# Kernel optimization log

Measured on AMD Instinct MI355X. Metric: run time of the kernel, lower is better.

The kernel has to match this reference:

```python
import jax, jax.numpy as jnp
import numpy as np

D_MODEL, D_STATE, D_CONV, EXPAND, L = 512, 16, 4, 2, 2048
D_INNER = EXPAND * D_MODEL


def _dwconv_causal(x, w, b):
    # x: (L, D), w: (D, K), b: (D,). torch Conv1d(groups=D, padding=K-1)[..., :L]
    K = w.shape[1]
    xp = jnp.pad(x, ((K - 1, 0), (0, 0)))
    windows = jnp.stack([xp[k:k + x.shape[0]] for k in range(K)], axis=-1)  # (L, D, K)
    return jnp.einsum('ldk,dk->ld', windows, w) + b


def _ssm_dir(x, inW, inb, cw, cb, xpW, xpb, dtW, dtb, outW, outb, A_log, Dp):
    xz = x @ inW + inb                      # (L, 2*Di)
    x_ssm, z = xz[:, :D_INNER], xz[:, D_INNER:]
    x_ssm = _dwconv_causal(x_ssm, cw, cb)   # (L, Di)
    sp = jax.nn.silu(x_ssm) @ xpW + xpb     # (L, Di + 2*S)
    delta = sp[:, :D_INNER]
    B = sp[:, D_INNER:D_INNER + D_STATE]
    C = sp[:, D_INNER + D_STATE:]
    dt = jax.nn.softplus(delta @ dtW + dtb)  # (L, Di)
    A = -jnp.exp(A_log)                      # (Di, S)
    dA = jnp.exp(dt[:, :, None] * A[None])                      # (L, Di, S)
    dBu = dt[:, :, None] * B[:, None, :] * x_ssm[:, :, None]    # (L, Di, S)

    def step(h, inp):
        a, bu = inp
        h = a * h + bu
        return h, h

    h0 = jnp.zeros((D_INNER, D_STATE), x.dtype)
    _, hs = jax.lax.scan(step, h0, (dA, dBu))   # (L, Di, S)
    y = jnp.einsum('lds,ls->ld', hs, C) + Dp * x_ssm
    return (y * jax.nn.silu(z)) @ outW + outb


def _make_params(key):
    ks = jax.random.split(key, 32)
    i = iter(range(32))
    def w(shape, scale=0.02):
        return (jax.random.normal(ks[next(i)], shape, jnp.float32) * scale)
    p = {}
    for pre in ('fwd_', 'bwd_'):
        p[pre + 'in_W'] = w((D_MODEL, 2 * D_INNER))
        p[pre + 'in_b'] = w((2 * D_INNER,))
        p[pre + 'conv_w'] = w((D_INNER, D_CONV), 0.1)
        p[pre + 'conv_b'] = w((D_INNER,))
        p[pre + 'xp_W'] = w((D_INNER, D_INNER + 2 * D_STATE))
        p[pre + 'xp_b'] = w((D_INNER + 2 * D_STATE,))
        p[pre + 'dt_W'] = w((D_INNER, D_INNER))
        p[pre + 'dt_b'] = w((D_INNER,))
        p[pre + 'out_W'] = w((D_INNER, D_MODEL))
        p[pre + 'out_b'] = w((D_MODEL,))
    p['A_log'] = jax.random.normal(ks[next(i)], (D_INNER, D_STATE), jnp.float32) * 0.5
    p['D_param'] = jnp.ones((D_INNER,), jnp.float32)
    p['fusion_W'] = w((2 * D_MODEL, D_MODEL))
    p['fusion_b'] = w((D_MODEL,))
    return p


def setup_inputs() -> dict:
    key = jax.random.key(0)
    kx, kp = jax.random.split(key)
    inp = {'x': jax.random.normal(kx, (L, D_MODEL), jnp.float32)}
    inp.update(_make_params(kp))
    return inp


def reference(x,
              fwd_in_W, fwd_in_b, fwd_conv_w, fwd_conv_b, fwd_xp_W, fwd_xp_b,
              fwd_dt_W, fwd_dt_b, fwd_out_W, fwd_out_b,
              bwd_in_W, bwd_in_b, bwd_conv_w, bwd_conv_b, bwd_xp_W, bwd_xp_b,
              bwd_dt_W, bwd_dt_b, bwd_out_W, bwd_out_b,
              A_log, D_param, fusion_W, fusion_b):
    out_fwd = _ssm_dir(x, fwd_in_W, fwd_in_b, fwd_conv_w, fwd_conv_b,
                       fwd_xp_W, fwd_xp_b, fwd_dt_W, fwd_dt_b,
                       fwd_out_W, fwd_out_b, A_log, D_param)
    out_bwd = _ssm_dir(x[::-1], bwd_in_W, bwd_in_b, bwd_conv_w, bwd_conv_b,
                       bwd_xp_W, bwd_xp_b, bwd_dt_W, bwd_dt_b,
                       bwd_out_W, bwd_out_b, A_log, D_param)[::-1]
    return jnp.concatenate([out_fwd, out_bwd], axis=-1) @ fusion_W + fusion_b
```

## Files before the change

kernel.cpp:

```cpp
#include <hip/hip_runtime.h>
#include <cmath>

#define L_SEQ 2048
#define DM 512
#define DI 1024
#define DS 16
#define NSP 1056
#define NC 64
#define CL 32

typedef unsigned short ushortT;
typedef unsigned int u32;
typedef __attribute__((ext_vector_type(8))) short short8;
typedef __attribute__((ext_vector_type(4))) float float4_t;
typedef __attribute__((address_space(1))) u32 gu32;
typedef __attribute__((address_space(3))) u32 lu32;

__device__ __forceinline__ float sigm(float x) { return 1.0f / (1.0f + __expf(-x)); }

__device__ __forceinline__ ushortT f2bf(float f) {
    unsigned u = __float_as_uint(f);
    unsigned r = u + 0x7FFFu + ((u >> 16) & 1u);
    return (ushortT)(r >> 16);
}

__device__ __forceinline__ void gl2lds16(const ushortT* g, ushortT* l) {
    __builtin_amdgcn_global_load_lds((gu32*)g, (lu32*)l, 16, 0, 0);
}

struct WC {
    const float* src[11];
    ushortT* dst[11];
    int ss[11], soff[11], ds_[11], tN[11], mode[11];
    int off[12];
};

__global__ __launch_bounds__(256) void wcvt_all(WC wc)
{
    __shared__ ushortT t[32][33];
    int b = blockIdx.x;
    int m = 0;
    while (b >= wc.off[m + 1]) ++m;
    int tl = b - wc.off[m];
    int n0 = (tl % wc.tN[m]) * 32;
    int k0 = (tl / wc.tN[m]) * 32;
    const float* W = wc.src[m];
    ushortT* D = wc.dst[m];
    int ss = wc.ss[m], soff = wc.soff[m], ds = wc.ds_[m];
    int tx = threadIdx.x & 31, ty = threadIdx.x >> 5;
    if (wc.mode[m] == 1) {
        #pragma unroll
        for (int i = 0; i < 32; i += 8)
            D[(size_t)(k0 + ty + i) * ds + n0 + tx] =
                f2bf(W[(size_t)(k0 + ty + i) * ss + soff + n0 + tx]);
    } else {
        #pragma unroll
        for (int i = 0; i < 32; i += 8)
            t[ty + i][tx] = f2bf(W[(size_t)(k0 + ty + i) * ss + soff + n0 + tx]);
        __syncthreads();
        #pragma unroll
        for (int i = 0; i < 32; i += 8)
            D[(size_t)(n0 + ty + i) * ds + k0 + tx] = t[tx][ty + i];
    }
}

__global__ __launch_bounds__(256) void bias_fold(
    const float* __restrict__ xpb0, const float* __restrict__ xpb1,
    const float* __restrict__ dtW0, const float* __restrict__ dtW1,
    const float* __restrict__ dtb0, const float* __restrict__ dtb1,
    const float* __restrict__ outb0, const float* __restrict__ outb1,
    const float* __restrict__ fuW, const float* __restrict__ fub,
    float* __restrict__ BFdt0, float* __restrict__ BFdt1, float* __restrict__ BFof)
{
    int idx = blockIdx.x * 256 + threadIdx.x;
    if (idx < 2112) {
        int dir = idx >= 1056;
        int m = idx - dir * 1056;
        const float* xpb = dir ? xpb1 : xpb0;
        float* BF = dir ? BFdt1 : BFdt0;
        if (m < 1024) {
            const float* dtW = dir ? dtW1 : dtW0;
            const float* dtb = dir ? dtb1 : dtb0;
            float acc = dtb[m];
            for (int n = 0; n < 1024; ++n) acc += xpb[n] * dtW[n * 1024 + m];
            BF[m] = acc;
        } else {
            BF[m] = xpb[m];
        }
    } else if (idx < 2624) {
        int n = idx - 2112;
        float acc = fub[n];
        for (int j = 0; j < 512; ++j)  acc += outb0[j] * fuW[j * 512 + n];
        for (int j = 0; j < 512; ++j)  acc += outb1[j] * fuW[(512 + j) * 512 + n];
        BFof[n] = acc;
    }
}

__global__ __launch_bounds__(256) void xcvt_k(const float* __restrict__ x,
                                              ushortT* __restrict__ xb, int n)
{
    int i = (blockIdx.x * 256 + threadIdx.x) * 4;
    if (i < n) {
        float4_t v = *(const float4_t*)(x + i);
        xb[i + 0] = f2bf(v[0]); xb[i + 1] = f2bf(v[1]);
        xb[i + 2] = f2bf(v[2]); xb[i + 3] = f2bf(v[3]);
    }
}

template<int BM, int BN>
__global__ __launch_bounds__(256) void gemm_bf16(
    const ushortT* __restrict__ A, int lda, long long Astr, int revAmode,
    const ushortT* __restrict__ W, long long Wstr,
    const float* __restrict__ bias0, const float* __restrict__ bias1,
    float* __restrict__ Cf, int ldcf, long long Cfstr,
    float* __restrict__ Cf2, int ldcf2, long long Cf2str, int Nsplit,
    ushortT* __restrict__ Cb, int ldcb, long long Cbstr,
    int M, int N, int K, int epi)
{
    const int dir = blockIdx.z;
    A  += (size_t)dir * Astr;
    W  += (size_t)dir * Wstr;
    if (Cf)  Cf  += (size_t)dir * Cfstr;
    if (Cf2) Cf2 += (size_t)dir * Cf2str;
    if (Cb)  Cb  += (size_t)dir * Cbstr;
    const float* bias = dir ? bias1 : bias0;
    const int revA = (revAmode == 2) ? dir : revAmode;

    constexpr int MI = BM / 32;
    constexpr int NI = BN / 32;
    constexpr int CA = BM / 64;
    constexpr int CB = BN / 64;

    __shared__ ushortT As[2][BM * 32];
    __shared__ ushortT Bs[2][BN * 32];

    const int tid  = threadIdx.x;
    const int wave = tid >> 6;
    const int lane = tid & 63;
    const int quad = lane >> 4;
    const int r    = lane & 15;
    const int wm   = (wave >> 1) * (BM / 2);
    const int wn   = (wave & 1) * (BN / 2);
    const int bm   = blockIdx.y * BM;
    const int bn   = blockIdx.x * BN;

    const int lrow = lane >> 2;
    const int lk   = (lane & 3) * 8;

    const ushortT* gA[CA];
    ushortT* lA[CA];
    #pragma unroll
    for (int c = 0; c < CA; ++c) {
        int row = bm + c * 64 + wave * 16 + lrow;
        if (revA) row = M - 1 - row;
        gA[c] = A + (size_t)row * lda + lk;
        lA[c] = &As[0][(c * 64 + wave * 16) * 32];
    }
    const ushortT* gB[CB];
    ushortT* lB[CB];
    #pragma unroll
    for (int c = 0; c < CB; ++c) {
        int row = bn + c * 64 + wave * 16 + lrow;
        if (row > N - 1) row = N - 1;
        gB[c] = W + (size_t)row * K + lk;
        lB[c] = &Bs[0][(c * 64 + wave * 16) * 32];
    }
    constexpr int ABUF = BM * 32;
    constexpr int BBUF = BN * 32;

    float4_t acc[MI][NI];
    #pragma unroll
    for (int i = 0; i < MI; ++i)
        #pragma unroll
        for (int j = 0; j < NI; ++j)
            acc[i][j] = (float4_t){0.f, 0.f, 0.f, 0.f};

    const int nsteps = K >> 5;

    #pragma unroll
    for (int c = 0; c < CA; ++c) gl2lds16(gA[c], lA[c]);
    #pragma unroll
    for (int c = 0; c < CB; ++c) gl2lds16(gB[c], lB[c]);

    for (int i = 0; i < nsteps; i += 2) {
        __syncthreads();
        {
            int kq = (i + 1) << 5;
            if (i + 1 < nsteps) {
                #pragma unroll
                for (int c = 0; c < CA; ++c) gl2lds16(gA[c] + kq, lA[c] + ABUF);
                #pragma unroll
                for (int c = 0; c < CB; ++c) gl2lds16(gB[c] + kq, lB[c] + BBUF);
            }
        }
        {
            short8 af[MI], bf[NI];
            #pragma unroll
            for (int mi = 0; mi < MI; ++mi)
                af[mi] = *(const short8*)&As[0][(wm + mi * 16 + r) * 32 + quad * 8];
            #pragma unroll
            for (int ni = 0; ni < NI; ++ni)
                bf[ni] = *(const short8*)&Bs[0][(wn + ni * 16 + r) * 32 + quad * 8];
            #pragma unroll
            for (int mi = 0; mi < MI; ++mi)
                #pragma unroll
                for (int ni = 0; ni < NI; ++ni)
                    acc[mi][ni] = __builtin_amdgcn_mfma_f32_16x16x32_bf16(
                        af[mi], bf[ni], acc[mi][ni], 0, 0, 0);
        }
        __syncthreads();
        {
            int kq = (i + 2) << 5;
            if (i + 2 < nsteps) {
                #pragma unroll
                for (int c = 0; c < CA; ++c) gl2lds16(gA[c] + kq, lA[c]);
                #pragma unroll
                for (int c = 0; c < CB; ++c) gl2lds16(gB[c] + kq, lB[c]);
            }
        }
        {
            short8 af[MI], bf[NI];
            #pragma unroll
            for (int mi = 0; mi < MI; ++mi)
                af[mi] = *(const short8*)&As[1][(wm + mi * 16 + r) * 32 + quad * 8];
            #pragma unroll
            for (int ni = 0; ni < NI; ++ni)
                bf[ni] = *(const short8*)&Bs[1][(wn + ni * 16 + r) * 32 + quad * 8];
            #pragma unroll
            for (int mi = 0; mi < MI; ++mi)
                #pragma unroll
                for (int ni = 0; ni < NI; ++ni)
                    acc[mi][ni] = __builtin_amdgcn_mfma_f32_16x16x32_bf16(
                        af[mi], bf[ni], acc[mi][ni], 0, 0, 0);
        }
    }

    #pragma unroll
    for (int mi = 0; mi < MI; ++mi) {
        int rowb = bm + wm + mi * 16 + quad * 4;
        #pragma unroll
        for (int ni = 0; ni < NI; ++ni) {
            int gn = bn + wn + ni * 16 + r;
            if (gn < N) {
                float bv = bias ? bias[gn] : 0.0f;
                #pragma unroll
                for (int j = 0; j < 4; ++j) {
                    int orow = rowb + j;
                    float v = acc[mi][ni][j] + bv;
                    if (epi == 1 && gn < Nsplit) v = (v > 20.0f) ? v : log1pf(__expf(v));
                    if (epi == 3) {
                        atomicAdd(&Cf[(size_t)orow * ldcf + gn], v);
                    } else {
                        if (gn < Nsplit) {
                            if (Cf) Cf[(size_t)orow * ldcf + gn] = v;
                        } else if (Cf2) {
                            Cf2[(size_t)orow * ldcf2 + gn - Nsplit] = v;
                        }
                        if (Cb) Cb[(size_t)orow * ldcb + gn] = f2bf(v);
                    }
                }
            }
        }
    }
}

__global__ __launch_bounds__(256) void conv_k(
    const float* __restrict__ XZ,
    const float* __restrict__ cw0, const float* __restrict__ cw1,
    const float* __restrict__ cb0, const float* __restrict__ cb1,
    float* __restrict__ XC, ushortT* __restrict__ SCb)
{
    int dir = blockIdx.z;
    XZ += (size_t)dir * L_SEQ * 2 * DI;
    XC += (size_t)dir * L_SEQ * DI;
    SCb += (size_t)dir * L_SEQ * DI;
    const float* cw = dir ? cw1 : cw0;
    const float* cb = dir ? cb1 : cb0;
    int idx = blockIdx.x * 256 + threadIdx.x;
    int d = idx & (DI - 1);
    int l = idx >> 10;
    float w0 = cw[d * 4 + 0], w1 = cw[d * 4 + 1], w2 = cw[d * 4 + 2], w3 = cw[d * 4 + 3];
    float acc = cb[d];
    if (l >= 3) acc += XZ[(size_t)(l - 3) * (2 * DI) + d] * w0;
    if (l >= 2) acc += XZ[(size_t)(l - 2) * (2 * DI) + d] * w1;
    if (l >= 1) acc += XZ[(size_t)(l - 1) * (2 * DI) + d] * w2;
    acc += XZ[(size_t)l * (2 * DI) + d] * w3;
    XC[idx] = acc;
    SCb[idx] = f2bf(acc * sigm(acc));
}

__global__ __launch_bounds__(256) void scanA_k(
    const float* __restrict__ DT, const float* __restrict__ XC,
    const float* __restrict__ BC, const float* __restrict__ Alog,
    float* __restrict__ Pend, float* __restrict__ Hl)
{
    __shared__ float Bsh[CL][DS];
    int dir = blockIdx.z;
    int c = blockIdx.y;
    int d = blockIdx.x * 256 + threadIdx.x;
    DT += (size_t)dir * L_SEQ * DI;
    XC += (size_t)dir * L_SEQ * DI;
    BC += (size_t)dir * L_SEQ * 32;
    int l0 = c * CL;
    for (int i = threadIdx.x; i < CL * DS; i += 256) {
        int ll = i >> 4, ss = i & 15;
        Bsh[ll][ss] = BC[(size_t)(l0 + ll) * 32 + ss];
    }
    __syncthreads();
    float Ae[DS], h[DS], P[DS];
    #pragma unroll
    for (int s = 0; s < DS; ++s) { Ae[s] = -__expf(Alog[d * DS + s]); h[s] = 0.f; P[s] = 1.f; }
    for (int t = 0; t < CL; ++t) {
        int l = l0 + t;
        float dt = DT[(size_t)l * DI + d];
        float xv = XC[(size_t)l * DI + d];
        float dtx = dt * xv;
        #pragma unroll
        for (int s = 0; s < DS; ++s) {
            float e = __expf(dt * Ae[s]);
            h[s] = e * h[s] + dtx * Bsh[t][s];
            P[s] *= e;
        }
    }
    size_t o = ((size_t)(dir * NC + c) * DI + d) * DS;
    #pragma unroll
    for (int s = 0; s < DS; ++s) { Pend[o + s] = P[s]; Hl[o + s] = h[s]; }
}

__global__ __launch_bounds__(256) void scanB_k(
    const float* __restrict__ Pend, const float* __restrict__ Hl, float* __restrict__ Hs)
{
    int idx = blockIdx.x * 256 + threadIdx.x;
    float h = 0.f;
    int ds = idx & 16383;
    int dir = idx >> 14;
    for (int c = 0; c < NC; ++c) {
        size_t o = ((size_t)(dir * NC + c)) * (DI * DS) + ds;
        Hs[o] = h;
        h = Pend[o] * h + Hl[o];
    }
}

__global__ __launch_bounds__(256) void scanC_k(
    const float* __restrict__ DT, const float* __restrict__ XC,
    const float* __restrict__ BC, const float* __restrict__ XZ,
    const float* __restrict__ Alog, const float* __restrict__ Dp,
    const float* __restrict__ Hs, ushortT* __restrict__ Gb)
{
    __shared__ float Bsh[CL][DS];
    __shared__ float Csh[CL][DS];
    int dir = blockIdx.z;
    int c = blockIdx.y;
    int d = blockIdx.x * 256 + threadIdx.x;
    DT += (size_t)dir * L_SEQ * DI;
    XC += (size_t)dir * L_SEQ * DI;
    BC += (size_t)dir * L_SEQ * 32;
    XZ += (size_t)dir * L_SEQ * (2 * DI);
    Gb += (size_t)dir * L_SEQ * DI;
    int l0 = c * CL;
    for (int i = threadIdx.x; i < CL * DS; i += 256) {
        int ll = i >> 4, ss = i & 15;
        size_t base = (size_t)(l0 + ll) * 32;
        Bsh[ll][ss] = BC[base + ss];
        Csh[ll][ss] = BC[base + DS + ss];
    }
    __syncthreads();
    float Ae[DS], h[DS];
    size_t o = ((size_t)(dir * NC + c) * DI + d) * DS;
    #pragma unroll
    for (int s = 0; s < DS; ++s) { Ae[s] = -__expf(Alog[d * DS + s]); h[s] = Hs[o + s]; }
    float dpv = Dp[d];
    for (int t = 0; t < CL; ++t) {
        int l = l0 + t;
        float dt = DT[(size_t)l * DI + d];
        float xv = XC[(size_t)l * DI + d];
        float dtx = dt * xv;
        float y = 0.f;
        #pragma unroll
        for (int s = 0; s < DS; ++s) {
            float e = __expf(dt * Ae[s]);
            h[s] = e * h[s] + dtx * Bsh[t][s];
            y += h[s] * Csh[t][s];
        }
        y += dpv * xv;
        float z = XZ[(size_t)l * (2 * DI) + DI + d];
        Gb[(size_t)l * DI + d] = f2bf(y * (z * sigm(z)));
    }
}

extern "C" void kernel_launch(void* const* d_in, const int* in_sizes, int n_in,
                              void* d_out, int out_size, void* d_ws, size_t ws_size,
                              hipStream_t stream)
{
    (void)in_sizes; (void)n_in; (void)out_size; (void)ws_size;
    const float* x = (const float*)d_in[0];
    const float* inW[2]  = {(const float*)d_in[1],  (const float*)d_in[11]};
    const float* inb[2]  = {(const float*)d_in[2],  (const float*)d_in[12]};
    const float* cw[2]   = {(const float*)d_in[3],  (const float*)d_in[13]};
    const float* cb[2]   = {(const float*)d_in[4],  (const float*)d_in[14]};
    const float* xpW[2]  = {(const float*)d_in[5],  (const float*)d_in[15]};
    const float* xpb[2]  = {(const float*)d_in[6],  (const float*)d_in[16]};
    const float* dtW[2]  = {(const float*)d_in[7],  (const float*)d_in[17]};
    const float* dtb[2]  = {(const float*)d_in[8],  (const float*)d_in[18]};
    const float* outW[2] = {(const float*)d_in[9],  (const float*)d_in[19]};
    const float* outb[2] = {(const float*)d_in[10], (const float*)d_in[20]};
    const float* Alog = (const float*)d_in[21];
    const float* Dp   = (const float*)d_in[22];
    const float* fuW  = (const float*)d_in[23];
    const float* fub  = (const float*)d_in[24];
    float* out = (float*)d_out;

    float* ws = (float*)d_ws;
    size_t off = 0;
    auto alloc = [&](size_t n) { float* p = ws + off; off += n; return p; };
    float* XZ   = alloc((size_t)2 * L_SEQ * 2 * DI);
    float* XC   = alloc((size_t)2 * L_SEQ * DI);
    float* DTb  = alloc((size_t)2 * L_SEQ * DI);
    float* BCf  = alloc((size_t)2 * L_SEQ * 32);
    float* Pend = alloc((size_t)2 * NC * DI * DS);
    float* Hl   = alloc((size_t)2 * NC * DI * DS);
    float* Hs   = alloc((size_t)2 * NC * DI * DS);
    float* BFdt0 = alloc(1056);
    float* BFdt1 = alloc(1056);
    float* BFof  = alloc(512);

    ushortT* wsu = (ushortT*)(ws + off);
    size_t uoff = 0;
    auto ualloc = [&](size_t n) { ushortT* p = wsu + uoff; uoff += n; return p; };
    ushortT* WtIn  = ualloc((size_t)2 * (2 * DI) * DM);
    ushortT* WtDt  = ualloc((size_t)2 * DI * DI);
    ushortT* WtFu  = ualloc((size_t)DM * DI);
    ushortT* WtXpF = ualloc((size_t)2 * NSP * DI);
    ushortT* XpD   = ualloc((size_t)2 * DI * DI);
    ushortT* OutC  = ualloc((size_t)2 * DI * DM);
    ushortT* WtOF  = ualloc((size_t)2 * DM * DI);
    ushortT* XB    = ualloc((size_t)L_SEQ * DM);
    ushortT* SCb   = ualloc((size_t)2 * L_SEQ * DI);
    ushortT* Gb    = ualloc((size_t)2 * L_SEQ * DI);

    dim3 blk(256);

    hipMemsetAsync(out, 0, (size_t)L_SEQ * DM * sizeof(float), stream);

    WC wc;
    struct E { const float* s; ushortT* d; int ss, so, ds, N, K, mode; };
    E es[11] = {
        {inW[0],  WtIn,                          2 * DI, 0,    DM, 2 * DI, DM, 0},
        {inW[1],  WtIn + (size_t)2 * DI * DM,    2 * DI, 0,    DM, 2 * DI, DM, 0},
        {dtW[0],  WtDt,                          DI,     0,    DI, DI,     DI, 0},
        {dtW[1],  WtDt + (size_t)DI * DI,        DI,     0,    DI, DI,     DI, 0},
        {fuW,     WtFu,                          DM,     0,    DI, DM,     DI, 0},
        {xpW[0],  WtXpF + (size_t)DI * DI,       NSP,    DI,   DI, 32,     DI, 0},
        {xpW[1],  WtXpF + (size_t)NSP * DI + (size_t)DI * DI, NSP, DI, DI, 32, DI, 0},
        {xpW[0],  XpD,                           NSP,    0,    DI, DI,     DI, 1},
        {xpW[1],  XpD + (size_t)DI * DI,         NSP,    0,    DI, DI,     DI, 1},
        {outW[0], OutC,                          DM,     0,    DM, DM,     DI, 1},
        {outW[1], OutC + (size_t)DI * DM,        DM,     0,    DM, DM,     DI, 1},
    };
    wc.off[0] = 0;
    for (int m = 0; m < 11; ++m) {
        wc.src[m] = es[m].s; wc.dst[m] = es[m].d;
        wc.ss[m] = es[m].ss; wc.soff[m] = es[m].so; wc.ds_[m] = es[m].ds;
        wc.tN[m] = es[m].N / 32; wc.mode[m] = es[m].mode;
        wc.off[m + 1] = wc.off[m] + (es[m].N / 32) * (es[m].K / 32);
    }
    wcvt_all<<<dim3(wc.off[11]), blk, 0, stream>>>(wc);
    xcvt_k<<<dim3(L_SEQ * DM / 1024), blk, 0, stream>>>(x, XB, L_SEQ * DM);
    bias_fold<<<dim3(11), blk, 0, stream>>>(
        xpb[0], xpb[1], dtW[0], dtW[1], dtb[0], dtb[1],
        outb[0], outb[1], fuW, fub, BFdt0, BFdt1, BFof);

    gemm_bf16<64, 64><<<dim3(16, 16, 2), blk, 0, stream>>>(
        WtDt, DI, (long long)DI * DI, 0, XpD, (long long)DI * DI,
        nullptr, nullptr, nullptr, 0, 0, nullptr, 0, 0, DI,
        WtXpF, DI, (long long)NSP * DI, DI, DI, DI, 0);
    gemm_bf16<64, 64><<<dim3(16, 8, 2), blk, 0, stream>>>(
        WtFu, DI, (long long)DM, 0, OutC, (long long)DI * DM,
        nullptr, nullptr, nullptr, 0, 0, nullptr, 0, 0, DI,
        WtOF, DI, (long long)DM * DI, DM, DI, DM, 0);

    gemm_bf16<64, 128><<<dim3(16, 32, 2), blk, 0, stream>>>(
        XB, DM, 0, 2, WtIn, (long long)2 * DI * DM, inb[0], inb[1],
        XZ, 2 * DI, (long long)L_SEQ * 2 * DI, nullptr, 0, 0, 2 * DI,
        nullptr, 0, 0, L_SEQ, 2 * DI, DM, 0);
    conv_k<<<dim3(L_SEQ * DI / 256, 1, 2), blk, 0, stream>>>(
        XZ, cw[0], cw[1], cb[0], cb[1], XC, SCb);
    gemm_bf16<64, 64><<<dim3((NSP + 63) / 64, 32, 2), blk, 0, stream>>>(
        SCb, DI, (long long)L_SEQ * DI, 0, WtXpF, (long long)NSP * DI, BFdt0, BFdt1,
        DTb, DI, (long long)L_SEQ * DI, BCf, 32, (long long)L_SEQ * 32, DI,
        nullptr, 0, 0, L_SEQ, NSP, DI, 1);
    scanA_k<<<dim3(DI / 256, NC, 2), blk, 0, stream>>>(DTb, XC, BCf, Alog, Pend, Hl);
    scanB_k<<<dim3(2 * DI * DS / 256), blk, 0, stream>>>(Pend, Hl, Hs);
    scanC_k<<<dim3(DI / 256, NC, 2), blk, 0, stream>>>(DTb, XC, BCf, XZ, Alog, Dp, Hs, Gb);
    gemm_bf16<64, 64><<<dim3(DM / 64, 32, 2), blk, 0, stream>>>(
        Gb, DI, (long long)L_SEQ * DI, 2, WtOF, (long long)DM * DI, BFof, nullptr,
        out, DM, 0, nullptr, 0, 0, DM,
        nullptr, 0, 0, L_SEQ, DM, DI, 3);
}
```

Measured before the change: 374.3 us.

## Parallelize bias folding per output and deepen GEMM K-tile to 64

```diff
diff --git a/kernel.cpp b/kernel.cpp
--- a/kernel.cpp
+++ b/kernel.cpp
@@ -72,27 +72,42 @@
     const float* __restrict__ fuW, const float* __restrict__ fub,
     float* __restrict__ BFdt0, float* __restrict__ BFdt1, float* __restrict__ BFof)
 {
-    int idx = blockIdx.x * 256 + threadIdx.x;
-    if (idx < 2112) {
-        int dir = idx >= 1056;
-        int m = idx - dir * 1056;
+    __shared__ float red[256];
+    int o = blockIdx.x;
+    int tid = threadIdx.x;
+    float acc = 0.0f;
+    if (o < 2112) {
+        int dir = o >= 1056;
+        int m = o - dir * 1056;
         const float* xpb = dir ? xpb1 : xpb0;
         float* BF = dir ? BFdt1 : BFdt0;
-        if (m < 1024) {
-            const float* dtW = dir ? dtW1 : dtW0;
-            const float* dtb = dir ? dtb1 : dtb0;
-            float acc = dtb[m];
-            for (int n = 0; n < 1024; ++n) acc += xpb[n] * dtW[n * 1024 + m];
-            BF[m] = acc;
-        } else {
-            BF[m] = xpb[m];
-        }
-    } else if (idx < 2624) {
-        int n = idx - 2112;
-        float acc = fub[n];
-        for (int j = 0; j < 512; ++j)  acc += outb0[j] * fuW[j * 512 + n];
-        for (int j = 0; j < 512; ++j)  acc += outb1[j] * fuW[(512 + j) * 512 + n];
-        BFof[n] = acc;
+        if (m >= 1024) {
+            if (tid == 0) BF[m] = xpb[m];
+            return;
+        }
+        const float* dtW = dir ? dtW1 : dtW0;
+        const float* dtb = dir ? dtb1 : dtb0;
+        for (int n = tid; n < 1024; n += 256) acc += xpb[n] * dtW[n * 1024 + m];
+        red[tid] = acc;
+        __syncthreads();
+        for (int s = 128; s > 0; s >>= 1) {
+            if (tid < s) red[tid] += red[tid + s];
+            __syncthreads();
+        }
+        if (tid == 0) BF[m] = red[0] + dtb[m];
+    } else {
+        int n = o - 2112;
+        for (int j = tid; j < 1024; j += 256) {
+            float ob = (j < 512) ? outb0[j] : outb1[j - 512];
+            acc += ob * fuW[(size_t)j * 512 + n];
+        }
+        red[tid] = acc;
+        __syncthreads();
+        for (int s = 128; s > 0; s >>= 1) {
+            if (tid < s) red[tid] += red[tid + s];
+            __syncthreads();
+        }
+        if (tid == 0) BFof[n] = red[0] + fub[n];
     }
 }
 
@@ -126,13 +141,14 @@
     const float* bias = dir ? bias1 : bias0;
     const int revA = (revAmode == 2) ? dir : revAmode;
 
+    constexpr int BK = 64;
     constexpr int MI = BM / 32;
     constexpr int NI = BN / 32;
-    constexpr int CA = BM / 64;
-    constexpr int CB = BN / 64;
-
-    __shared__ ushortT As[2][BM * 32];
-    __shared__ ushortT Bs[2][BN * 32];
+    constexpr int CA = BM / 32;
+    constexpr int CB = BN / 32;
+
+    __shared__ ushortT As[2][BM * BK];
+    __shared__ ushortT Bs[2][BN * BK];
 
     const int tid  = threadIdx.x;
     const int wave = tid >> 6;
@@ -144,29 +160,29 @@
     const int bm   = blockIdx.y * BM;
     const int bn   = blockIdx.x * BN;
 
-    const int lrow = lane >> 2;
-    const int lk   = (lane & 3) * 8;
+    const int lrow = lane >> 3;
+    const int lk   = (lane & 7) * 8;
 
     const ushortT* gA[CA];
     ushortT* lA[CA];
     #pragma unroll
     for (int c = 0; c < CA; ++c) {
-        int row = bm + c * 64 + wave * 16 + lrow;
+        int row = bm + c * 32 + wave * 8 + lrow;
         if (revA) row = M - 1 - row;
         gA[c] = A + (size_t)row * lda + lk;
-        lA[c] = &As[0][(c * 64 + wave * 16) * 32];
+        lA[c] = &As[0][(c * 32 + wave * 8) * BK];
     }
     const ushortT* gB[CB];
     ushortT* lB[CB];
     #pragma unroll
     for (int c = 0; c < CB; ++c) {
-        int row = bn + c * 64 + wave * 16 + lrow;
+        int row = bn + c * 32 + wave * 8 + lrow;
         if (row > N - 1) row = N - 1;
         gB[c] = W + (size_t)row * K + lk;
-        lB[c] = &Bs[0][(c * 64 + wave * 16) * 32];
-    }
-    constexpr int ABUF = BM * 32;
-    constexpr int BBUF = BN * 32;
+        lB[c] = &Bs[0][(c * 32 + wave * 8) * BK];
+    }
+    constexpr int ABUF = BM * BK;
+    constexpr int BBUF = BN * BK;
 
     float4_t acc[MI][NI];
     #pragma unroll
@@ -175,7 +191,7 @@
         for (int j = 0; j < NI; ++j)
             acc[i][j] = (float4_t){0.f, 0.f, 0.f, 0.f};
 
-    const int nsteps = K >> 5;
+    const int nsteps = K >> 6;
 
     #pragma unroll
     for (int c = 0; c < CA; ++c) gl2lds16(gA[c], lA[c]);
@@ -185,7 +201,7 @@
     for (int i = 0; i < nsteps; i += 2) {
         __syncthreads();
         {
-            int kq = (i + 1) << 5;
+            int kq = (i + 1) << 6;
             if (i + 1 < nsteps) {
                 #pragma unroll
                 for (int c = 0; c < CA; ++c) gl2lds16(gA[c] + kq, lA[c] + ABUF);
@@ -193,14 +209,15 @@
                 for (int c = 0; c < CB; ++c) gl2lds16(gB[c] + kq, lB[c] + BBUF);
             }
         }
-        {
+        #pragma unroll
+        for (int kh = 0; kh < 2; ++kh) {
             short8 af[MI], bf[NI];
             #pragma unroll
             for (int mi = 0; mi < MI; ++mi)
-                af[mi] = *(const short8*)&As[0][(wm + mi * 16 + r) * 32 + quad * 8];
+                af[mi] = *(const short8*)&As[0][(wm + mi * 16 + r) * BK + kh * 32 + quad * 8];
             #pragma unroll
             for (int ni = 0; ni < NI; ++ni)
-                bf[ni] = *(const short8*)&Bs[0][(wn + ni * 16 + r) * 32 + quad * 8];
+                bf[ni] = *(const short8*)&Bs[0][(wn + ni * 16 + r) * BK + kh * 32 + quad * 8];
             #pragma unroll
             for (int mi = 0; mi < MI; ++mi)
                 #pragma unroll
@@ -210,7 +227,7 @@
         }
         __syncthreads();
         {
-            int kq = (i + 2) << 5;
+            int kq = (i + 2) << 6;
             if (i + 2 < nsteps) {
                 #pragma unroll
                 for (int c = 0; c < CA; ++c) gl2lds16(gA[c] + kq, lA[c]);
@@ -218,14 +235,15 @@
                 for (int c = 0; c < CB; ++c) gl2lds16(gB[c] + kq, lB[c]);
             }
         }
-        {
+        #pragma unroll
+        for (int kh = 0; kh < 2; ++kh) {
             short8 af[MI], bf[NI];
             #pragma unroll
             for (int mi = 0; mi < MI; ++mi)
-                af[mi] = *(const short8*)&As[1][(wm + mi * 16 + r) * 32 + quad * 8];
+                af[mi] = *(const short8*)&As[1][(wm + mi * 16 + r) * BK + kh * 32 + quad * 8];
             #pragma unroll
             for (int ni = 0; ni < NI; ++ni)
-                bf[ni] = *(const short8*)&Bs[1][(wn + ni * 16 + r) * 32 + quad * 8];
+                bf[ni] = *(const short8*)&Bs[1][(wn + ni * 16 + r) * BK + kh * 32 + quad * 8];
             #pragma unroll
             for (int mi = 0; mi < MI; ++mi)
                 #pragma unroll
@@ -466,7 +484,7 @@
     }
     wcvt_all<<<dim3(wc.off[11]), blk, 0, stream>>>(wc);
     xcvt_k<<<dim3(L_SEQ * DM / 1024), blk, 0, stream>>>(x, XB, L_SEQ * DM);
-    bias_fold<<<dim3(11), blk, 0, stream>>>(
+    bias_fold<<<dim3(2624), blk, 0, stream>>>(
         xpb[0], xpb[1], dtW[0], dtW[1], dtb[0], dtb[1],
         outb[0], outb[1], fuW, fub, BFdt0, BFdt1, BFof);
 
```

After: 348.3 us. 1.07x faster.
